# Kernel optimization log

Hardware: AMD Instinct MI355X
Metric: run time of the kernel (lower is better)

The kernel has to match this reference:

```python
import jax, jax.numpy as jnp
import numpy as np

WS = 16            # window height = width
DIM = 512          # channels
H = 16             # num heads
HD = DIM // H      # head dim = 32
NW = 64            # num windows per image (mask leading dim)
B_ = 256           # num_windows * batch
N_IN = 512         # pre-stride sequence length
SCALE = HD ** -0.5
MAX_SEQ = 512
STRIDE = 2


def _relative_position_index(wh, ww):
    coords = np.stack(np.meshgrid(np.arange(wh), np.arange(ww), indexing='ij'))  # (2, wh, ww)
    cf = coords.reshape(2, -1)                             # (2, wh*ww)
    rc = (cf[:, :, None] - cf[:, None, :]).transpose(1, 2, 0).astype(np.int32)
    rc[:, :, 0] += wh - 1
    rc[:, :, 1] += ww - 1
    rc[:, :, 0] *= 2 * ww - 1
    return rc.sum(-1)                                      # (wh*ww, wh*ww)


def setup_inputs() -> dict:
    key = jax.random.key(0)
    ks = jax.random.split(key, 8)
    x = jax.random.normal(ks[0], (B_, N_IN, DIM), dtype=jnp.float32)
    y = jax.random.normal(ks[1], (B_, N_IN, DIM), dtype=jnp.float32)
    mask = jax.random.normal(ks[2], (NW, WS * WS, WS * WS), dtype=jnp.float32)
    q_w = jax.random.normal(ks[3], (DIM, DIM), dtype=jnp.float32) * 0.02
    q_b = jnp.zeros((DIM,), dtype=jnp.float32)
    kv_w = jax.random.normal(ks[4], (2 * DIM, DIM), dtype=jnp.float32) * 0.02
    kv_b = jnp.zeros((2 * DIM,), dtype=jnp.float32)
    proj_w = jax.random.normal(ks[5], (DIM, DIM), dtype=jnp.float32) * 0.02
    proj_b = jnp.zeros((DIM,), dtype=jnp.float32)
    bias_table = jax.random.normal(ks[6], ((2 * WS - 1) ** 2, H), dtype=jnp.float32) * 0.02
    rel_pos_index = jnp.asarray(_relative_position_index(WS, WS))  # (256, 256) int32
    return {"x": x, "y": y, "mask": mask, "q_w": q_w, "q_b": q_b,
            "kv_w": kv_w, "kv_b": kv_b, "proj_w": proj_w, "proj_b": proj_b,
            "bias_table": bias_table, "rel_pos_index": rel_pos_index}


def reference(x, y, mask, q_w, q_b, kv_w, kv_b, proj_w, proj_b, bias_table, rel_pos_index):
    # truncate + stride (as in forward)
    x = x[:, :MAX_SEQ][:, ::STRIDE]          # (B_, N, C), N = 256
    y = y[:, :MAX_SEQ][:, ::STRIDE]
    b, n, c = x.shape
    # projections
    q = (x @ q_w.T + q_b).reshape(b, n, H, HD).transpose(0, 2, 1, 3)   # (B_, H, N, D)
    kv = y @ kv_w.T + kv_b                                              # (B_, N, 2C)
    k = kv[..., :DIM].reshape(b, n, H, HD).transpose(0, 2, 1, 3)
    v = kv[..., DIM:].reshape(b, n, H, HD).transpose(0, 2, 1, 3)
    # scores
    attn = jnp.einsum('bhnd,bhmd->bhnm', q * SCALE, k)                  # (B_, H, N, N)
    # gathered relative position bias: (N, N, H) -> (H, N, N)
    rpb = bias_table[rel_pos_index].transpose(2, 0, 1)
    attn = attn + rpb[None]
    # window mask: view (B_//nW, nW, H, N, N) + mask[None,:,None]
    attn = attn.reshape(b // NW, NW, H, n, n) + mask[None, :, None]
    attn = attn.reshape(b, H, n, n)
    attn = jax.nn.softmax(attn, axis=-1)
    out = jnp.einsum('bhnm,bhmd->bhnd', attn, v)                        # (B_, H, N, D)
    out = out.transpose(0, 2, 1, 3).reshape(b, n, DIM)
    out = out @ proj_w.T + proj_b
    return out
```

## Files before the change

kernel.cpp:

```cpp
#include <hip/hip_runtime.h>

typedef _Float16 half8 __attribute__((ext_vector_type(8)));
typedef _Float16 half4 __attribute__((ext_vector_type(4)));
typedef _Float16 half2v __attribute__((ext_vector_type(2)));
typedef float f32x4 __attribute__((ext_vector_type(4)));

#define LOG2E 1.4426950408889634f
#define QSCALE (0.17677669529663687f * 1.4426950408889634f)

static __device__ __forceinline__ half4 cvt4h(float4 v) {
    half2v a = __builtin_bit_cast(half2v, __builtin_amdgcn_cvt_pkrtz(v.x, v.y));
    half2v b = __builtin_bit_cast(half2v, __builtin_amdgcn_cvt_pkrtz(v.z, v.w));
    return half4{ a[0], a[1], b[0], b[1] };
}

#define NB_X 16384
#define NB_Y 16384
#define NB_W 512
#define NB_M 4096
#define NB_R 4096

__global__ __launch_bounds__(256) void convert_kernel(
    const float* __restrict__ x, const float* __restrict__ y,
    const float* __restrict__ q_w, const float* __restrict__ kv_w,
    const float* __restrict__ proj_w, const float* __restrict__ mask,
    const float* __restrict__ table, const int* __restrict__ rpi,
    _Float16* __restrict__ Xh, _Float16* __restrict__ Yh,
    _Float16* __restrict__ Wh, _Float16* __restrict__ maskh,
    _Float16* __restrict__ rpbh)
{
    const int blk = blockIdx.x, t = threadIdx.x;
    if (blk < NB_X + NB_Y) {
        const float* src; _Float16* dst; int v;
        if (blk < NB_X) { v = blk * 256 + t; src = x; dst = Xh; }
        else { v = (blk - NB_X) * 256 + t; src = y; dst = Yh; }
        int r = v >> 6, ks = (v & 63) * 8;
        const float* s = src + ((size_t)(r >> 8) * 512 + (size_t)((r & 255) * 2)) * 512 + ks;
        half4 h0 = cvt4h(*(const float4*)s);
        half4 h1 = cvt4h(*(const float4*)(s + 4));
        half8 hv = { h0[0], h0[1], h0[2], h0[3], h1[0], h1[1], h1[2], h1[3] };
        *(half8*)(dst + (size_t)v * 8) = hv;
    } else if (blk < NB_X + NB_Y + NB_W) {
        int v = (blk - NB_X - NB_Y) * 256 + t;
        int row = v >> 6, ks = (v & 63) * 8;
        const float* s; float sc = 1.0f;
        if (row < 512)       { s = q_w + (size_t)row * 512;            sc = QSCALE; }
        else if (row < 1536) { s = kv_w + (size_t)(row - 512) * 512; }
        else                 { s = proj_w + (size_t)(row - 1536) * 512; }
        float4 a = *(const float4*)(s + ks);
        float4 b = *(const float4*)(s + ks + 4);
        a.x *= sc; a.y *= sc; a.z *= sc; a.w *= sc;
        b.x *= sc; b.y *= sc; b.z *= sc; b.w *= sc;
        half4 h0 = cvt4h(a), h1 = cvt4h(b);
        half8 hv = { h0[0], h0[1], h0[2], h0[3], h1[0], h1[1], h1[2], h1[3] };
        *(half8*)(Wh + (size_t)v * 8) = hv;
    } else if (blk < NB_X + NB_Y + NB_W + NB_M) {
        int i = (blk - NB_X - NB_Y - NB_W) * 256 + t;
        float4 v = ((const float4*)mask)[i];
        half4 hv = { (_Float16)(v.x * LOG2E), (_Float16)(v.y * LOG2E),
                     (_Float16)(v.z * LOG2E), (_Float16)(v.w * LOG2E) };
        *(half4*)(maskh + (size_t)i * 4) = hv;
    } else {
        int i = (blk - NB_X - NB_Y - NB_W - NB_M) * 256 + t;
        int p = i & 65535, hh = i >> 16;
        rpbh[i] = (_Float16)(table[rpi[p] * 16 + hh] * LOG2E);
    }
}

__global__ __launch_bounds__(256) void gemm_f16(
    const _Float16* __restrict__ Ah, const _Float16* __restrict__ Wh,
    const float* __restrict__ bias, float bscale,
    _Float16* __restrict__ qout, _Float16* __restrict__ kout,
    _Float16* __restrict__ vout, float* __restrict__ fout,
    int mode, int nct_sh)
{
    __shared__ __align__(16) _Float16 S[128 * 128];
    _Float16* As = S;
    _Float16* Ws = S + 128 * 64;
    const int nwg = gridDim.x;
    const int chunk = nwg >> 3;
    const int f = blockIdx.x;
    const int swz = (f & 7) * chunk + (f >> 3);
    const int ct = swz & ((1 << nct_sh) - 1);
    const int rt = swz >> nct_sh;

    const int t = threadIdx.x;
    const int lane = t & 63, wave = t >> 6;
    const int ql = lane & 15, g = lane >> 4;
    const int wr = (wave >> 1) * 64, wc = (wave & 1) * 64;

    const int sr = t >> 3;
    const int st = t & 7;
    const _Float16* aR = Ah + ((size_t)(rt * 128 + sr)) * 512 + st * 8;
    const _Float16* wR = Wh + ((size_t)(ct * 128 + sr)) * 512 + st * 8;
    char* asw = (char*)As + sr * 128 + ((st ^ (sr & 7)) << 4);
    char* wsw = (char*)Ws + sr * 128 + ((st ^ (sr & 7)) << 4);

    half8 a0 = *(const half8*)(aR);
    half8 a1 = *(const half8*)(aR + 32 * 512);
    half8 a2 = *(const half8*)(aR + 64 * 512);
    half8 a3 = *(const half8*)(aR + 96 * 512);
    half8 w0 = *(const half8*)(wR);
    half8 w1 = *(const half8*)(wR + 32 * 512);
    half8 w2 = *(const half8*)(wR + 64 * 512);
    half8 w3 = *(const half8*)(wR + 96 * 512);

    f32x4 acc[4][4] = {};
    for (int kk = 0; kk < 8; ++kk) {
        if (kk) __syncthreads();
        *(half8*)(asw)           = a0;
        *(half8*)(asw + 32*128)  = a1;
        *(half8*)(asw + 64*128)  = a2;
        *(half8*)(asw + 96*128)  = a3;
        *(half8*)(wsw)           = w0;
        *(half8*)(wsw + 32*128)  = w1;
        *(half8*)(wsw + 64*128)  = w2;
        *(half8*)(wsw + 96*128)  = w3;
        __syncthreads();
        if (kk < 7) {
            const int k0n = (kk + 1) * 64;
            a0 = *(const half8*)(aR + k0n);
            a1 = *(const half8*)(aR + 32 * 512 + k0n);
            a2 = *(const half8*)(aR + 64 * 512 + k0n);
            a3 = *(const half8*)(aR + 96 * 512 + k0n);
            w0 = *(const half8*)(wR + k0n);
            w1 = *(const half8*)(wR + 32 * 512 + k0n);
            w2 = *(const half8*)(wR + 64 * 512 + k0n);
            w3 = *(const half8*)(wR + 96 * 512 + k0n);
        }
#pragma unroll
        for (int kh = 0; kh < 2; ++kh) {
            half8 af[4], bf[4];
#pragma unroll
            for (int i = 0; i < 4; ++i) {
                int row = wr + i * 16 + ql;
                af[i] = *(const half8*)((const char*)As + row * 128 +
                        (((kh * 4 + g) ^ (ql & 7)) << 4));
            }
#pragma unroll
            for (int j = 0; j < 4; ++j) {
                int row = wc + j * 16 + ql;
                bf[j] = *(const half8*)((const char*)Ws + row * 128 +
                        (((kh * 4 + g) ^ (ql & 7)) << 4));
            }
#pragma unroll
            for (int i = 0; i < 4; ++i)
#pragma unroll
                for (int j = 0; j < 4; ++j)
                    acc[i][j] = __builtin_amdgcn_mfma_f32_16x16x32_f16(af[i], bf[j], acc[i][j], 0, 0, 0);
        }
    }

    if (mode == 2) {
#pragma unroll
        for (int j = 0; j < 4; ++j) {
            int c = ct * 128 + wc + j * 16 + ql;
            float bv = bias[c];
#pragma unroll
            for (int i = 0; i < 4; ++i)
#pragma unroll
                for (int rr = 0; rr < 4; ++rr) {
                    int r = rt * 128 + wr + i * 16 + g * 4 + rr;
                    fout[(size_t)r * 512 + c] = acc[i][j][rr] + bv;
                }
        }
        return;
    }

    __syncthreads();
#pragma unroll
    for (int j = 0; j < 4; ++j) {
        int col = wc + j * 16 + ql;
        float bv = bias[ct * 128 + col] * bscale;
#pragma unroll
        for (int i = 0; i < 4; ++i) {
#pragma unroll
            for (int rr = 0; rr < 4; ++rr) {
                int row = wr + i * 16 + g * 4 + rr;
                int scol = col ^ (((row >> 2) & 3) << 4);
                S[row * 128 + scol] = (_Float16)(acc[i][j][rr] + bv);
            }
        }
    }
    __syncthreads();
    {
        const int c0 = ct * 128 + wave * 32;
        const int b = (rt * 128) >> 8, n0 = (rt * 128) & 255;
        _Float16* dst;
        int cc = c0;
        if (mode == 0) { dst = qout; }
        else if (c0 < 512) { dst = kout; }
        else { dst = vout; cc = c0 - 512; }
        const int hw = cc >> 5;
        _Float16* gb = dst + ((size_t)(b * 16 + hw) * 256 + n0) * 32;
        const int dq = (lane & 3) * 8;
#pragma unroll
        for (int m = 0; m < 8; ++m) {
            int n = m * 16 + (lane >> 2);
            int colb = wave * 32 + dq;
            int scol = colb ^ (((n >> 2) & 3) << 4);
            half8 v = *(const half8*)(S + n * 128 + scol);
            *(half8*)(gb + (size_t)n * 32 + dq) = v;
        }
    }
}

__global__ __launch_bounds__(256, 2) void attn_kernel(
    const _Float16* __restrict__ Q, const _Float16* __restrict__ K,
    const _Float16* __restrict__ V, const _Float16* __restrict__ rpbh,
    const _Float16* __restrict__ maskh, _Float16* __restrict__ pre)
{
    __shared__ __align__(16) _Float16 bias_s[2][16 * 256];
    const int blk = blockIdx.x;
    const int w = blk >> 4, h = blk & 15;
    const int t = threadIdx.x;
    const int lane = t & 63, wave = t >> 6;
    const int ql = lane & 15, g = lane >> 4;
    const int b = w + 64 * wave;
    const size_t blk_b = (size_t)(b * 16 + h) * 8192;
    const _Float16* Qp = Q + blk_b + g * 8;
    const _Float16* Kp = K + blk_b + ql * 32 + g * 8;
    const _Float16* rp = rpbh + (size_t)h * 65536;
    const _Float16* mp = maskh + (size_t)w * 65536;

    half8 karr[16];
#pragma unroll
    for (int tt = 0; tt < 16; ++tt)
        karr[tt] = *(const half8*)(Kp + tt * 512);

    half4 vf0[16], vf1[16];
    {
        const _Float16* vb = V + blk_b + g * 128 + ql;
#pragma unroll
        for (int tt = 0; tt < 16; ++tt) {
#pragma unroll
            for (int j = 0; j < 4; ++j) {
                vf0[tt][j] = vb[tt * 512 + j * 32];
                vf1[tt][j] = vb[tt * 512 + j * 32 + 16];
            }
        }
    }

    const int sq = t >> 4;
    const int scb = (t & 15) * 32;
    const int sw = sq << 3;
    const int sgoff = (t & 15) * 16;

    {
        const _Float16* rrow = rp + (size_t)sq * 256 + sgoff;
        const _Float16* mrow = mp + (size_t)sq * 256 + sgoff;
        half8 s0 = *(const half8*)rrow + *(const half8*)mrow;
        half8 s1 = *(const half8*)(rrow + 8) + *(const half8*)(mrow + 8);
        char* sb = (char*)bias_s[0] + sq * 512;
        *(half4*)(sb + ((scb) ^ sw))      = __builtin_shufflevector(s0, s0, 0, 1, 2, 3);
        *(half4*)(sb + ((scb + 8) ^ sw))  = __builtin_shufflevector(s0, s0, 4, 5, 6, 7);
        *(half4*)(sb + ((scb + 16) ^ sw)) = __builtin_shufflevector(s1, s1, 0, 1, 2, 3);
        *(half4*)(sb + ((scb + 24) ^ sw)) = __builtin_shufflevector(s1, s1, 4, 5, 6, 7);
    }
    __syncthreads();

#pragma unroll 1
    for (int qg = 0; qg < 16; ++qg) {
        const int q0 = qg * 16;
        half8 nr0, nm0, nr1, nm1;
        if (qg < 15) {
            const _Float16* rrow = rp + (size_t)(q0 + 16 + sq) * 256 + sgoff;
            const _Float16* mrow = mp + (size_t)(q0 + 16 + sq) * 256 + sgoff;
            nr0 = *(const half8*)rrow;
            nm0 = *(const half8*)mrow;
            nr1 = *(const half8*)(rrow + 8);
            nm1 = *(const half8*)(mrow + 8);
        }

        const int q = q0 + ql;
        half8 qf = *(const half8*)(Qp + (size_t)q * 32);
        const char* bb = (const char*)bias_s[qg & 1] + ql * 512;
        f32x4 lsum = { 0.f, 0.f, 0.f, 0.f };
        f32x4 o0 = { 0.f, 0.f, 0.f, 0.f }, o1 = { 0.f, 0.f, 0.f, 0.f };
#pragma unroll
        for (int tt = 0; tt < 16; ++tt) {
            half4 bs = *(const half4*)(bb + ((tt * 32 + g * 8) ^ (ql << 3)));
            f32x4 bf = { (float)bs[0], (float)bs[1], (float)bs[2], (float)bs[3] };
            f32x4 s = __builtin_amdgcn_mfma_f32_16x16x32_f16(karr[tt], qf, bf, 0, 0, 0);
            float e0 = __builtin_amdgcn_exp2f(s[0]);
            float e1 = __builtin_amdgcn_exp2f(s[1]);
            float e2 = __builtin_amdgcn_exp2f(s[2]);
            float e3 = __builtin_amdgcn_exp2f(s[3]);
            lsum[0] += e0; lsum[1] += e1; lsum[2] += e2; lsum[3] += e3;
            half2v p01 = __builtin_bit_cast(half2v, __builtin_amdgcn_cvt_pkrtz(e0, e1));
            half2v p23 = __builtin_bit_cast(half2v, __builtin_amdgcn_cvt_pkrtz(e2, e3));
            half4 pf = { p01[0], p01[1], p23[0], p23[1] };
            o0 = __builtin_amdgcn_mfma_f32_16x16x16f16(pf, vf0[tt], o0, 0, 0, 0);
            o1 = __builtin_amdgcn_mfma_f32_16x16x16f16(pf, vf1[tt], o1, 0, 0, 0);
        }
        float l = (lsum[0] + lsum[1]) + (lsum[2] + lsum[3]);
        l += __shfl_xor(l, 16);
        l += __shfl_xor(l, 32);
#pragma unroll
        for (int rr = 0; rr < 4; ++rr) {
            float inv = __builtin_amdgcn_rcpf(__shfl(l, g * 4 + rr));
            int row = q0 + g * 4 + rr;
            size_t ob = ((size_t)b * 256 + row) * 512 + h * 32;
            pre[ob + ql] = (_Float16)(o0[rr] * inv);
            pre[ob + 16 + ql] = (_Float16)(o1[rr] * inv);
        }
        if (qg < 15) {
            half8 s0 = nr0 + nm0, s1 = nr1 + nm1;
            char* sb = (char*)bias_s[(qg + 1) & 1] + sq * 512;
            *(half4*)(sb + ((scb) ^ sw))      = __builtin_shufflevector(s0, s0, 0, 1, 2, 3);
            *(half4*)(sb + ((scb + 8) ^ sw))  = __builtin_shufflevector(s0, s0, 4, 5, 6, 7);
            *(half4*)(sb + ((scb + 16) ^ sw)) = __builtin_shufflevector(s1, s1, 0, 1, 2, 3);
            *(half4*)(sb + ((scb + 24) ^ sw)) = __builtin_shufflevector(s1, s1, 4, 5, 6, 7);
        }
        __syncthreads();
    }
}

extern "C" void kernel_launch(void* const* d_in, const int* in_sizes, int n_in,
                              void* d_out, int out_size, void* d_ws, size_t ws_size,
                              hipStream_t stream)
{
    const float* x      = (const float*)d_in[0];
    const float* y      = (const float*)d_in[1];
    const float* mask   = (const float*)d_in[2];
    const float* q_w    = (const float*)d_in[3];
    const float* q_b    = (const float*)d_in[4];
    const float* kv_w   = (const float*)d_in[5];
    const float* kv_b   = (const float*)d_in[6];
    const float* proj_w = (const float*)d_in[7];
    const float* proj_b = (const float*)d_in[8];
    const float* btab   = (const float*)d_in[9];
    const int*   rpi    = (const int*)d_in[10];
    float* out = (float*)d_out;

    char* ws = (char*)d_ws;
    _Float16* XK  = (_Float16*)(ws);
    _Float16* YP  = (_Float16*)(ws + ((size_t)64 << 20));
    _Float16* Qw  = (_Float16*)(ws + ((size_t)128 << 20));
    _Float16* Vw  = (_Float16*)(ws + ((size_t)192 << 20));
    _Float16* Wh  = (_Float16*)(ws + ((size_t)256 << 20));
    _Float16* Rpb = (_Float16*)(ws + ((size_t)258 << 20));
    _Float16* Mh  = (_Float16*)(ws + ((size_t)260 << 20));

    convert_kernel<<<NB_X + NB_Y + NB_W + NB_M + NB_R, 256, 0, stream>>>(
        x, y, q_w, kv_w, proj_w, mask, btab, rpi, XK, YP, Wh, Mh, Rpb);
    gemm_f16<<<2048, 256, 0, stream>>>(XK, Wh, q_b, QSCALE,
                                       Qw, nullptr, nullptr, nullptr, 0, 2);
    gemm_f16<<<4096, 256, 0, stream>>>(YP, Wh + 512 * 512, kv_b, 1.0f,
                                       nullptr, XK, Vw, nullptr, 1, 3);
    attn_kernel<<<1024, 256, 0, stream>>>(Qw, XK, Vw, Rpb, Mh, YP);
    gemm_f16<<<2048, 256, 0, stream>>>(YP, Wh + 1536 * 512, proj_b, 1.0f,
                                       nullptr, nullptr, nullptr, out, 2, 2);
}
```

Before: 415.6 us.

## Pre-swizzle weights into MFMA fragment layout and load B directly from global

The weight matrices are stored in a blocked layout that matches the MFMA B-fragment order, so each wave reads its B operands straight from global memory (mostly L2 hits) into registers. The weight tile no longer passes through LDS, which removes half the LDS writes and reads per k-step and frees shared memory. The cost is uncoalesced-free but unprefetched global loads issued right before use, which may expose latency inside the k-loop.

After: 459.9 us. 10.7% more time.

```diff
diff --git a/kernel.cpp b/kernel.cpp
--- a/kernel.cpp
+++ b/kernel.cpp
@@ -26,7 +26,7 @@
     const float* __restrict__ proj_w, const float* __restrict__ mask,
     const float* __restrict__ table, const int* __restrict__ rpi,
     _Float16* __restrict__ Xh, _Float16* __restrict__ Yh,
-    _Float16* __restrict__ Wh, _Float16* __restrict__ maskh,
+    _Float16* __restrict__ Wt, _Float16* __restrict__ maskh,
     _Float16* __restrict__ rpbh)
 {
     const int blk = blockIdx.x, t = threadIdx.x;
@@ -42,18 +42,19 @@
         *(half8*)(dst + (size_t)v * 8) = hv;
     } else if (blk < NB_X + NB_Y + NB_W) {
         int v = (blk - NB_X - NB_Y) * 256 + t;
-        int row = v >> 6, ks = (v & 63) * 8;
+        int row = v >> 6, c8 = v & 63;
         const float* s; float sc = 1.0f;
         if (row < 512)       { s = q_w + (size_t)row * 512;            sc = QSCALE; }
         else if (row < 1536) { s = kv_w + (size_t)(row - 512) * 512; }
         else                 { s = proj_w + (size_t)(row - 1536) * 512; }
-        float4 a = *(const float4*)(s + ks);
-        float4 b = *(const float4*)(s + ks + 4);
+        float4 a = *(const float4*)(s + c8 * 8);
+        float4 b = *(const float4*)(s + c8 * 8 + 4);
         a.x *= sc; a.y *= sc; a.z *= sc; a.w *= sc;
         b.x *= sc; b.y *= sc; b.z *= sc; b.w *= sc;
         half4 h0 = cvt4h(a), h1 = cvt4h(b);
         half8 hv = { h0[0], h0[1], h0[2], h0[3], h1[0], h1[1], h1[2], h1[3] };
-        *(half8*)(Wh + (size_t)v * 8) = hv;
+        int off = (row >> 4) * 8192 + (c8 >> 2) * 512 + ((c8 & 3) * 16 + (row & 15)) * 8;
+        *(half8*)(Wt + off) = hv;
     } else if (blk < NB_X + NB_Y + NB_W + NB_M) {
         int i = (blk - NB_X - NB_Y - NB_W) * 256 + t;
         float4 v = ((const float4*)mask)[i];
@@ -68,15 +69,14 @@
 }
 
 __global__ __launch_bounds__(256) void gemm_f16(
-    const _Float16* __restrict__ Ah, const _Float16* __restrict__ Wh,
+    const _Float16* __restrict__ Ah, const _Float16* __restrict__ Wt,
     const float* __restrict__ bias, float bscale,
     _Float16* __restrict__ qout, _Float16* __restrict__ kout,
     _Float16* __restrict__ vout, float* __restrict__ fout,
-    int mode, int nct_sh)
+    int mode, int nct_sh, int nbo)
 {
     __shared__ __align__(16) _Float16 S[128 * 128];
     _Float16* As = S;
-    _Float16* Ws = S + 128 * 64;
     const int nwg = gridDim.x;
     const int chunk = nwg >> 3;
     const int f = blockIdx.x;
@@ -92,18 +92,19 @@
     const int sr = t >> 3;
     const int st = t & 7;
     const _Float16* aR = Ah + ((size_t)(rt * 128 + sr)) * 512 + st * 8;
-    const _Float16* wR = Wh + ((size_t)(ct * 128 + sr)) * 512 + st * 8;
     char* asw = (char*)As + sr * 128 + ((st ^ (sr & 7)) << 4);
-    char* wsw = (char*)Ws + sr * 128 + ((st ^ (sr & 7)) << 4);
+
+    const _Float16* wtp[4];
+#pragma unroll
+    for (int j = 0; j < 4; ++j) {
+        int nb = nbo + ct * 8 + (wc >> 4) + j;
+        wtp[j] = Wt + (size_t)nb * 8192 + lane * 8;
+    }
 
     half8 a0 = *(const half8*)(aR);
     half8 a1 = *(const half8*)(aR + 32 * 512);
     half8 a2 = *(const half8*)(aR + 64 * 512);
     half8 a3 = *(const half8*)(aR + 96 * 512);
-    half8 w0 = *(const half8*)(wR);
-    half8 w1 = *(const half8*)(wR + 32 * 512);
-    half8 w2 = *(const half8*)(wR + 64 * 512);
-    half8 w3 = *(const half8*)(wR + 96 * 512);
 
     f32x4 acc[4][4] = {};
     for (int kk = 0; kk < 8; ++kk) {
@@ -112,25 +113,23 @@
         *(half8*)(asw + 32*128)  = a1;
         *(half8*)(asw + 64*128)  = a2;
         *(half8*)(asw + 96*128)  = a3;
-        *(half8*)(wsw)           = w0;
-        *(half8*)(wsw + 32*128)  = w1;
-        *(half8*)(wsw + 64*128)  = w2;
-        *(half8*)(wsw + 96*128)  = w3;
         __syncthreads();
+        half8 wf0[4], wf1[4];
+#pragma unroll
+        for (int j = 0; j < 4; ++j) {
+            wf0[j] = *(const half8*)(wtp[j] + kk * 1024);
+            wf1[j] = *(const half8*)(wtp[j] + kk * 1024 + 512);
+        }
         if (kk < 7) {
             const int k0n = (kk + 1) * 64;
             a0 = *(const half8*)(aR + k0n);
             a1 = *(const half8*)(aR + 32 * 512 + k0n);
             a2 = *(const half8*)(aR + 64 * 512 + k0n);
             a3 = *(const half8*)(aR + 96 * 512 + k0n);
-            w0 = *(const half8*)(wR + k0n);
-            w1 = *(const half8*)(wR + 32 * 512 + k0n);
-            w2 = *(const half8*)(wR + 64 * 512 + k0n);
-            w3 = *(const half8*)(wR + 96 * 512 + k0n);
         }
 #pragma unroll
         for (int kh = 0; kh < 2; ++kh) {
-            half8 af[4], bf[4];
+            half8 af[4];
 #pragma unroll
             for (int i = 0; i < 4; ++i) {
                 int row = wr + i * 16 + ql;
@@ -138,16 +137,11 @@
                         (((kh * 4 + g) ^ (ql & 7)) << 4));
             }
 #pragma unroll
-            for (int j = 0; j < 4; ++j) {
-                int row = wc + j * 16 + ql;
-                bf[j] = *(const half8*)((const char*)Ws + row * 128 +
-                        (((kh * 4 + g) ^ (ql & 7)) << 4));
-            }
-#pragma unroll
             for (int i = 0; i < 4; ++i)
 #pragma unroll
                 for (int j = 0; j < 4; ++j)
-                    acc[i][j] = __builtin_amdgcn_mfma_f32_16x16x32_f16(af[i], bf[j], acc[i][j], 0, 0, 0);
+                    acc[i][j] = __builtin_amdgcn_mfma_f32_16x16x32_f16(
+                        af[i], kh ? wf1[j] : wf0[j], acc[i][j], 0, 0, 0);
         }
     }
 
@@ -338,17 +332,17 @@
     _Float16* YP  = (_Float16*)(ws + ((size_t)64 << 20));
     _Float16* Qw  = (_Float16*)(ws + ((size_t)128 << 20));
     _Float16* Vw  = (_Float16*)(ws + ((size_t)192 << 20));
-    _Float16* Wh  = (_Float16*)(ws + ((size_t)256 << 20));
+    _Float16* Wt  = (_Float16*)(ws + ((size_t)256 << 20));
     _Float16* Rpb = (_Float16*)(ws + ((size_t)258 << 20));
     _Float16* Mh  = (_Float16*)(ws + ((size_t)260 << 20));
 
     convert_kernel<<<NB_X + NB_Y + NB_W + NB_M + NB_R, 256, 0, stream>>>(
-        x, y, q_w, kv_w, proj_w, mask, btab, rpi, XK, YP, Wh, Mh, Rpb);
-    gemm_f16<<<2048, 256, 0, stream>>>(XK, Wh, q_b, QSCALE,
-                                       Qw, nullptr, nullptr, nullptr, 0, 2);
-    gemm_f16<<<4096, 256, 0, stream>>>(YP, Wh + 512 * 512, kv_b, 1.0f,
-                                       nullptr, XK, Vw, nullptr, 1, 3);
+        x, y, q_w, kv_w, proj_w, mask, btab, rpi, XK, YP, Wt, Mh, Rpb);
+    gemm_f16<<<2048, 256, 0, stream>>>(XK, Wt, q_b, QSCALE,
+                                       Qw, nullptr, nullptr, nullptr, 0, 2, 0);
+    gemm_f16<<<4096, 256, 0, stream>>>(YP, Wt, kv_b, 1.0f,
+                                       nullptr, XK, Vw, nullptr, 1, 3, 32);
     attn_kernel<<<1024, 256, 0, stream>>>(Qw, XK, Vw, Rpb, Mh, YP);
-    gemm_f16<<<2048, 256, 0, stream>>>(YP, Wh + 1536 * 512, proj_b, 1.0f,
-                                       nullptr, nullptr, nullptr, out, 2, 2);
-}
+    gemm_f16<<<2048, 256, 0, stream>>>(YP, Wt, proj_b, 1.0f,
+                                       nullptr, nullptr, nullptr, out, 2, 2, 96);
+}
```

## Merge Q and KV projection GEMMs into one launch; stage attention output via LDS

Applied to the files above, without the earlier changes.

Refactors the GEMM body into a device function and adds a merged kernel that runs the Q projection and KV projection as one 6144-block launch. This removes a launch boundary and the tail between them, and it needs a separate K buffer, so the workspace layout grows with a fallback path when the workspace is small. Attention output is now written through a swizzled LDS tile and stored as 16-byte vectors instead of scattered 2-byte stores. The trade-off is extra LDS use in the attention kernel and a dependence on a larger workspace.

After: 432.2 us. 1.04x slower.

```diff
diff --git a/kernel.cpp b/kernel.cpp
--- a/kernel.cpp
+++ b/kernel.cpp
@@ -67,19 +67,17 @@
     }
 }
 
-__global__ __launch_bounds__(256) void gemm_f16(
-    const _Float16* __restrict__ Ah, const _Float16* __restrict__ Wh,
+static __device__ __forceinline__ void gemm_core(
+    _Float16* S, int f, int nwg,
+    const _Float16* __restrict__ Ah, const _Float16* __restrict__ Whp,
     const float* __restrict__ bias, float bscale,
     _Float16* __restrict__ qout, _Float16* __restrict__ kout,
     _Float16* __restrict__ vout, float* __restrict__ fout,
     int mode, int nct_sh)
 {
-    __shared__ __align__(16) _Float16 S[128 * 128];
     _Float16* As = S;
     _Float16* Ws = S + 128 * 64;
-    const int nwg = gridDim.x;
     const int chunk = nwg >> 3;
-    const int f = blockIdx.x;
     const int swz = (f & 7) * chunk + (f >> 3);
     const int ct = swz & ((1 << nct_sh) - 1);
     const int rt = swz >> nct_sh;
@@ -92,7 +90,7 @@
     const int sr = t >> 3;
     const int st = t & 7;
     const _Float16* aR = Ah + ((size_t)(rt * 128 + sr)) * 512 + st * 8;
-    const _Float16* wR = Wh + ((size_t)(ct * 128 + sr)) * 512 + st * 8;
+    const _Float16* wR = Whp + ((size_t)(ct * 128 + sr)) * 512 + st * 8;
     char* asw = (char*)As + sr * 128 + ((st ^ (sr & 7)) << 4);
     char* wsw = (char*)Ws + sr * 128 + ((st ^ (sr & 7)) << 4);
 
@@ -205,12 +203,41 @@
     }
 }
 
+__global__ __launch_bounds__(256) void gemm_f16(
+    const _Float16* __restrict__ Ah, const _Float16* __restrict__ Whp,
+    const float* __restrict__ bias, float bscale,
+    _Float16* __restrict__ qout, _Float16* __restrict__ kout,
+    _Float16* __restrict__ vout, float* __restrict__ fout,
+    int mode, int nct_sh)
+{
+    __shared__ __align__(16) _Float16 S[128 * 128];
+    gemm_core(S, blockIdx.x, gridDim.x, Ah, Whp, bias, bscale,
+              qout, kout, vout, fout, mode, nct_sh);
+}
+
+__global__ __launch_bounds__(256) void qkv_merged(
+    const _Float16* __restrict__ Xh, const _Float16* __restrict__ Yh,
+    const _Float16* __restrict__ Wh, const float* __restrict__ q_b,
+    const float* __restrict__ kv_b, _Float16* __restrict__ Qw,
+    _Float16* __restrict__ Kw, _Float16* __restrict__ Vw)
+{
+    __shared__ __align__(16) _Float16 S[128 * 128];
+    const int f = blockIdx.x;
+    if (f < 2048)
+        gemm_core(S, f, 2048, Xh, Wh, q_b, QSCALE,
+                  Qw, nullptr, nullptr, nullptr, 0, 2);
+    else
+        gemm_core(S, f - 2048, 4096, Yh, Wh + 512 * 512, kv_b, 1.0f,
+                  nullptr, Kw, Vw, nullptr, 1, 3);
+}
+
 __global__ __launch_bounds__(256, 2) void attn_kernel(
     const _Float16* __restrict__ Q, const _Float16* __restrict__ K,
     const _Float16* __restrict__ V, const _Float16* __restrict__ rpbh,
     const _Float16* __restrict__ maskh, _Float16* __restrict__ pre)
 {
     __shared__ __align__(16) _Float16 bias_s[2][16 * 256];
+    __shared__ __align__(16) _Float16 ox[4][512];
     const int blk = blockIdx.x;
     const int w = blk >> 4, h = blk & 15;
     const int t = threadIdx.x;
@@ -296,14 +323,23 @@
         float l = (lsum[0] + lsum[1]) + (lsum[2] + lsum[3]);
         l += __shfl_xor(l, 16);
         l += __shfl_xor(l, 32);
+
+        _Float16* oxw = ox[wave];
 #pragma unroll
         for (int rr = 0; rr < 4; ++rr) {
             float inv = __builtin_amdgcn_rcpf(__shfl(l, g * 4 + rr));
-            int row = q0 + g * 4 + rr;
-            size_t ob = ((size_t)b * 256 + row) * 512 + h * 32;
-            pre[ob + ql] = (_Float16)(o0[rr] * inv);
-            pre[ob + 16 + ql] = (_Float16)(o1[rr] * inv);
-        }
+            int lr = g * 4 + rr;
+            oxw[lr * 32 + ((((ql >> 3) ^ g) << 3) | (ql & 7))] =
+                (_Float16)(o0[rr] * inv);
+            oxw[lr * 32 + (((((ql >> 3) + 2) ^ g) << 3) | (ql & 7))] =
+                (_Float16)(o1[rr] * inv);
+        }
+        half8 vv = *(const half8*)(oxw + (lane >> 2) * 32 +
+                                   ((lane & 3) ^ (lane >> 4)) * 8);
+        size_t ob2 = ((size_t)b * 256 + q0 + (lane >> 2)) * 512 + h * 32 +
+                     (lane & 3) * 8;
+        *(half8*)(pre + ob2) = vv;
+
         if (qg < 15) {
             half8 s0 = nr0 + nm0, s1 = nr1 + nm1;
             char* sb = (char*)bias_s[(qg + 1) & 1] + sq * 512;
@@ -334,21 +370,39 @@
     float* out = (float*)d_out;
 
     char* ws = (char*)d_ws;
-    _Float16* XK  = (_Float16*)(ws);
-    _Float16* YP  = (_Float16*)(ws + ((size_t)64 << 20));
-    _Float16* Qw  = (_Float16*)(ws + ((size_t)128 << 20));
-    _Float16* Vw  = (_Float16*)(ws + ((size_t)192 << 20));
-    _Float16* Wh  = (_Float16*)(ws + ((size_t)256 << 20));
-    _Float16* Rpb = (_Float16*)(ws + ((size_t)258 << 20));
-    _Float16* Mh  = (_Float16*)(ws + ((size_t)260 << 20));
-
-    convert_kernel<<<NB_X + NB_Y + NB_W + NB_M + NB_R, 256, 0, stream>>>(
-        x, y, q_w, kv_w, proj_w, mask, btab, rpi, XK, YP, Wh, Mh, Rpb);
-    gemm_f16<<<2048, 256, 0, stream>>>(XK, Wh, q_b, QSCALE,
-                                       Qw, nullptr, nullptr, nullptr, 0, 2);
-    gemm_f16<<<4096, 256, 0, stream>>>(YP, Wh + 512 * 512, kv_b, 1.0f,
-                                       nullptr, XK, Vw, nullptr, 1, 3);
-    attn_kernel<<<1024, 256, 0, stream>>>(Qw, XK, Vw, Rpb, Mh, YP);
-    gemm_f16<<<2048, 256, 0, stream>>>(YP, Wh + 1536 * 512, proj_b, 1.0f,
-                                       nullptr, nullptr, nullptr, out, 2, 2);
-}
+    if (ws_size >= ((size_t)332 << 20)) {
+        _Float16* Xh  = (_Float16*)(ws);
+        _Float16* YP  = (_Float16*)(ws + ((size_t)64 << 20));
+        _Float16* Qw  = (_Float16*)(ws + ((size_t)128 << 20));
+        _Float16* Kw  = (_Float16*)(ws + ((size_t)192 << 20));
+        _Float16* Vw  = (_Float16*)(ws + ((size_t)256 << 20));
+        _Float16* Wh  = (_Float16*)(ws + ((size_t)320 << 20));
+        _Float16* Rpb = (_Float16*)(ws + ((size_t)322 << 20));
+        _Float16* Mh  = (_Float16*)(ws + ((size_t)324 << 20));
+
+        convert_kernel<<<NB_X + NB_Y + NB_W + NB_M + NB_R, 256, 0, stream>>>(
+            x, y, q_w, kv_w, proj_w, mask, btab, rpi, Xh, YP, Wh, Mh, Rpb);
+        qkv_merged<<<6144, 256, 0, stream>>>(Xh, YP, Wh, q_b, kv_b, Qw, Kw, Vw);
+        attn_kernel<<<1024, 256, 0, stream>>>(Qw, Kw, Vw, Rpb, Mh, YP);
+        gemm_f16<<<2048, 256, 0, stream>>>(YP, Wh + 1536 * 512, proj_b, 1.0f,
+                                           nullptr, nullptr, nullptr, out, 2, 2);
+    } else {
+        _Float16* XK  = (_Float16*)(ws);
+        _Float16* YP  = (_Float16*)(ws + ((size_t)64 << 20));
+        _Float16* Qw  = (_Float16*)(ws + ((size_t)128 << 20));
+        _Float16* Vw  = (_Float16*)(ws + ((size_t)192 << 20));
+        _Float16* Wh  = (_Float16*)(ws + ((size_t)256 << 20));
+        _Float16* Rpb = (_Float16*)(ws + ((size_t)258 << 20));
+        _Float16* Mh  = (_Float16*)(ws + ((size_t)260 << 20));
+
+        convert_kernel<<<NB_X + NB_Y + NB_W + NB_M + NB_R, 256, 0, stream>>>(
+            x, y, q_w, kv_w, proj_w, mask, btab, rpi, XK, YP, Wh, Mh, Rpb);
+        gemm_f16<<<2048, 256, 0, stream>>>(XK, Wh, q_b, QSCALE,
+                                           Qw, nullptr, nullptr, nullptr, 0, 2);
+        gemm_f16<<<4096, 256, 0, stream>>>(YP, Wh + 512 * 512, kv_b, 1.0f,
+                                           nullptr, XK, Vw, nullptr, 1, 3);
+        attn_kernel<<<1024, 256, 0, stream>>>(Qw, XK, Vw, Rpb, Mh, YP);
+        gemm_f16<<<2048, 256, 0, stream>>>(YP, Wh + 1536 * 512, proj_b, 1.0f,
+                                           nullptr, nullptr, nullptr, out, 2, 2);
+    }
+}
```
